# Performance work log

Measured on AMD Instinct MI355X. Metric: run time of the kernel, lower is better.

Reference implementation:

```python
import jax, jax.numpy as jnp
import numpy as np

B, M, N, K = 64, 1024, 1024, 128


def setup_inputs() -> dict:
    key = jax.random.key(0)
    k1, k2 = jax.random.split(key)
    # int8 operands in [-128, 127]; stored as int8 like the CUDA kernel expects
    a = jax.random.randint(k1, (B, M, K), -128, 128, dtype=jnp.int32).astype(jnp.int8)
    b = jax.random.randint(k2, (B, N, K), -128, 128, dtype=jnp.int32).astype(jnp.int8)
    # alpha = a_scale * b_scale / output_scale (scalar buffer 'a' in the module)
    alpha = jnp.float32(0.0078125)
    return {"a": a, "b": b, "alpha": alpha}


def reference(a, b, alpha):
    acc = jnp.einsum("bmk,bnk->bmn", a.astype(jnp.int32), b.astype(jnp.int32))  # [B,M,N] int32
    # fused epilogue: scale by alpha, round-to-nearest, store as int32 (s32t output)
    return jnp.round(acc.astype(jnp.float32) * alpha).astype(jnp.int32)
```

## Files before the change

kernel.cpp:

```cpp
#include <hip/hip_runtime.h>
#include <stdint.h>


typedef int v4i  __attribute__((ext_vector_type(4)));
typedef int v16i __attribute__((ext_vector_type(16)));

__device__ __forceinline__ int pack4(v4i w) {
    return (w.x & 0xFF) | ((w.y & 0xFF) << 8) | ((w.z & 0xFF) << 16) | (w.w << 24);
}

__device__ __forceinline__ void lgkm_barrier() {
    asm volatile("s_waitcnt lgkmcnt(0)" ::: "memory");
    __builtin_amdgcn_s_barrier();
}

__global__ __launch_bounds__(256) void prepack_kernel(
    const int* __restrict__ A, const int* __restrict__ Bm,
    uint8_t* __restrict__ Apk, uint8_t* __restrict__ Bpk)
{
    const int g = blockIdx.x * 256 + threadIdx.x;
    const size_t eoff = (size_t)g * 16;

    v4i a[4], b[4];
#pragma unroll
    for (int i = 0; i < 4; ++i) {
        a[i] = __builtin_nontemporal_load((const v4i*)(A + eoff) + i);
        b[i] = __builtin_nontemporal_load((const v4i*)(Bm + eoff) + i);
    }
    v4i pa = { pack4(a[0]), pack4(a[1]), pack4(a[2]), pack4(a[3]) };
    v4i pb = { pack4(b[0]), pack4(b[1]), pack4(b[2]), pack4(b[3]) };
    *(v4i*)(Apk + eoff) = pa;
    *(v4i*)(Bpk + eoff) = pb;
}

__global__ __launch_bounds__(256, 4) void bmm_s8s8_s32_kernel(
    const uint8_t* __restrict__ Apk,
    const uint8_t* __restrict__ Bpk,
    const float*   __restrict__ alpha_p,
    int*           __restrict__ out)
{
    __shared__ uint8_t smem[32768];
    uint8_t* Als = smem;
    uint8_t* Bls = smem + 16384;

    const int tid   = threadIdx.x;
    const int lane  = tid & 63;
    const int wave  = tid >> 6;
    const int half_ = lane >> 5;
    const int lrow  = lane & 31;

    const int bz = blockIdx.z;
    const int m0 = blockIdx.y << 7;
    const int n0 = blockIdx.x << 7;

    const float alpha = *alpha_p;

    const size_t abase = ((size_t)bz * 1024 + (size_t)m0) * 128;
    const size_t bbase = ((size_t)bz * 1024 + (size_t)n0) * 128;

    v4i pa[4], pb[4];
#pragma unroll
    for (int t = 0; t < 4; ++t) {
        const int G = t * 256 + tid;
        pa[t] = *(const v4i*)(Apk + abase + (size_t)G * 16);
        pb[t] = *(const v4i*)(Bpk + bbase + (size_t)G * 16);
    }
#pragma unroll
    for (int t = 0; t < 4; ++t) {
        const int G  = t * 256 + tid;
        const int m  = G >> 3;
        const int gp = G & 7;
        const int loff = m * 128 + ((gp ^ (m & 7)) << 4);
        *(v4i*)(Als + loff) = pa[t];
        *(v4i*)(Bls + loff) = pb[t];
    }
    lgkm_barrier();

    v16i acc[4] = {};
#pragma unroll
    for (int kk = 0; kk < 4; ++kk) {
        const int g = kk * 2 + half_;
        const int n = wave * 32 + lrow;
        const v4i bf = *(const v4i*)(Bls + n * 128 + ((g ^ (n & 7)) << 4));
        v4i af[4];
#pragma unroll
        for (int mi = 0; mi < 4; ++mi) {
            const int m = mi * 32 + lrow;
            af[mi] = *(const v4i*)(Als + m * 128 + ((g ^ (m & 7)) << 4));
        }
#pragma unroll
        for (int mi = 0; mi < 4; ++mi)
            acc[mi] = __builtin_amdgcn_mfma_i32_32x32x32_i8(af[mi], bf, acc[mi], 0, 0, 0);
    }
    lgkm_barrier();

    int* chunk = (int*)smem;
    int* outb  = out + ((size_t)bz << 20) + n0;

#pragma unroll
    for (int J = 0; J < 2; ++J) {
#pragma unroll
        for (int q = 0; q < 2; ++q) {
#pragma unroll
            for (int r = 0; r < 16; ++r) {
                const int row_local = q * 32 + (r & 3) + 8 * (r >> 2) + 4 * half_;
                chunk[row_local * 128 + wave * 32 + lrow] =
                    __float2int_rn((float)acc[2 * J + q][r] * alpha);
            }
        }
        lgkm_barrier();
#pragma unroll
        for (int p = 0; p < 8; ++p) {
            const int row_local = p * 8 + (tid >> 5);
            const v4i v = *(const v4i*)((const uint8_t*)chunk + p * 4096 + tid * 16);
            *(v4i*)(outb + (size_t)(m0 + J * 64 + row_local) * 1024 + (tid & 31) * 4) = v;
        }
        if (J == 0) lgkm_barrier();
    }
}

extern "C" void kernel_launch(void* const* d_in, const int* in_sizes, int n_in,
                              void* d_out, int out_size, void* d_ws, size_t ws_size,
                              hipStream_t stream) {
    const int*   A     = (const int*)d_in[0];
    const int*   Bm    = (const int*)d_in[1];
    const float* alpha = (const float*)d_in[2];
    int*         out   = (int*)d_out;

    uint8_t* Apk = (uint8_t*)d_ws;
    uint8_t* Bpk = (uint8_t*)d_ws + (8u << 20);

    prepack_kernel<<<dim3(2048), dim3(256), 0, stream>>>(A, Bm, Apk, Bpk);

    dim3 grid(8, 8, 64);
    bmm_s8s8_s32_kernel<<<grid, dim3(256), 0, stream>>>(Apk, Bpk, alpha, out);
}
```

Measured before the change: 327.9 us.

## Fuse int32-to-int8 packing into the batched GEMM kernel load stage

Removes the separate prepack kernel and its workspace write and read. The GEMM blocks now load the int32 operands directly, pack them to int8 in registers and store them into the swizzled LDS layout with 4-byte writes. This saves one launch and the packed-buffer round trip through memory. In exchange, each tile reload pulls four times as many bytes from global memory, since every A and B tile is re-read by 8 blocks, and the kernel issues more LDS store instructions.

```diff
diff --git a/kernel.cpp b/kernel.cpp
--- a/kernel.cpp
+++ b/kernel.cpp
@@ -14,30 +14,11 @@
     __builtin_amdgcn_s_barrier();
 }
 
-__global__ __launch_bounds__(256) void prepack_kernel(
-    const int* __restrict__ A, const int* __restrict__ Bm,
-    uint8_t* __restrict__ Apk, uint8_t* __restrict__ Bpk)
-{
-    const int g = blockIdx.x * 256 + threadIdx.x;
-    const size_t eoff = (size_t)g * 16;
-
-    v4i a[4], b[4];
-#pragma unroll
-    for (int i = 0; i < 4; ++i) {
-        a[i] = __builtin_nontemporal_load((const v4i*)(A + eoff) + i);
-        b[i] = __builtin_nontemporal_load((const v4i*)(Bm + eoff) + i);
-    }
-    v4i pa = { pack4(a[0]), pack4(a[1]), pack4(a[2]), pack4(a[3]) };
-    v4i pb = { pack4(b[0]), pack4(b[1]), pack4(b[2]), pack4(b[3]) };
-    *(v4i*)(Apk + eoff) = pa;
-    *(v4i*)(Bpk + eoff) = pb;
-}
-
-__global__ __launch_bounds__(256, 4) void bmm_s8s8_s32_kernel(
-    const uint8_t* __restrict__ Apk,
-    const uint8_t* __restrict__ Bpk,
-    const float*   __restrict__ alpha_p,
-    int*           __restrict__ out)
+__global__ __launch_bounds__(256, 4) void bmm_s8s8_s32_fused(
+    const int*   __restrict__ A32,
+    const int*   __restrict__ B32,
+    const float* __restrict__ alpha_p,
+    int*         __restrict__ out)
 {
     __shared__ uint8_t smem[32768];
     uint8_t* Als = smem;
@@ -55,24 +36,27 @@
 
     const float alpha = *alpha_p;
 
-    const size_t abase = ((size_t)bz * 1024 + (size_t)m0) * 128;
-    const size_t bbase = ((size_t)bz * 1024 + (size_t)n0) * 128;
+    const int* Ap = A32 + ((size_t)bz * 1024 + (size_t)m0) * 128;
+    const int* Bp = B32 + ((size_t)bz * 1024 + (size_t)n0) * 128;
 
-    v4i pa[4], pb[4];
 #pragma unroll
-    for (int t = 0; t < 4; ++t) {
-        const int G = t * 256 + tid;
-        pa[t] = *(const v4i*)(Apk + abase + (size_t)G * 16);
-        pb[t] = *(const v4i*)(Bpk + bbase + (size_t)G * 16);
-    }
+    for (int t = 0; t < 16; t += 2) {
+        v4i a_[2], b_[2];
 #pragma unroll
-    for (int t = 0; t < 4; ++t) {
-        const int G  = t * 256 + tid;
-        const int m  = G >> 3;
-        const int gp = G & 7;
-        const int loff = m * 128 + ((gp ^ (m & 7)) << 4);
-        *(v4i*)(Als + loff) = pa[t];
-        *(v4i*)(Bls + loff) = pb[t];
+        for (int j = 0; j < 2; ++j) {
+            const int G = (t + j) * 256 + tid;
+            a_[j] = *((const v4i*)Ap + G);
+            b_[j] = *((const v4i*)Bp + G);
+        }
+#pragma unroll
+        for (int j = 0; j < 2; ++j) {
+            const int G = (t + j) * 256 + tid;
+            const int m = G >> 5;
+            const int q = G & 31;
+            const int loff = m * 128 + (((q >> 2) ^ (m & 7)) << 4) + ((q & 3) << 2);
+            *(int*)(Als + loff) = pack4(a_[j]);
+            *(int*)(Bls + loff) = pack4(b_[j]);
+        }
     }
     lgkm_barrier();
 
@@ -126,12 +110,8 @@
     const int*   Bm    = (const int*)d_in[1];
     const float* alpha = (const float*)d_in[2];
     int*         out   = (int*)d_out;
-
-    uint8_t* Apk = (uint8_t*)d_ws;
-    uint8_t* Bpk = (uint8_t*)d_ws + (8u << 20);
-
-    prepack_kernel<<<dim3(2048), dim3(256), 0, stream>>>(A, Bm, Apk, Bpk);
+    (void)d_ws; (void)ws_size;
 
     dim3 grid(8, 8, 64);
-    bmm_s8s8_s32_kernel<<<grid, dim3(256), 0, stream>>>(Apk, Bpk, alpha, out);
+    bmm_s8s8_s32_fused<<<grid, dim3(256), 0, stream>>>(A, Bm, alpha, out);
 }
```

Measured after the change: 342.5 us. +4.5%, slower.
